# Kernel tuning notes

Measured on AMD Instinct MI355X. Metric: run time of the kernel, lower is better.

## Reference

```python
import jax, jax.numpy as jnp
import numpy as np

DEPTH, BREADTH, N_HEADS = 6, 1024, 16
D_HEAD = BREADTH // N_HEADS
EPS = 1e-5


def layer_norm(x, g, b):
    m = jnp.mean(x, axis=-1, keepdims=True)
    v = jnp.mean(jnp.square(x - m), axis=-1, keepdims=True)
    return (x - m) * jax.lax.rsqrt(v + EPS) * g + b


def setup_inputs() -> dict:
    key = jax.random.key(0)
    ks = jax.random.split(key, 16)
    B, S, Dm, Dff = 4, 1024, BREADTH, 4 * BREADTH
    s = 0.02
    return {
        "x": jax.random.normal(ks[0], (B, S, Dm), dtype=jnp.float32),
        "mask": jnp.ones((B, S, S), dtype=jnp.int32),
        "wq": s * jax.random.normal(ks[1], (DEPTH, Dm, Dm), dtype=jnp.float32),
        "bq": jnp.zeros((DEPTH, Dm), dtype=jnp.float32),
        "wk": s * jax.random.normal(ks[2], (DEPTH, Dm, Dm), dtype=jnp.float32),
        "bk": jnp.zeros((DEPTH, Dm), dtype=jnp.float32),
        "wv": s * jax.random.normal(ks[3], (DEPTH, Dm, Dm), dtype=jnp.float32),
        "bv": jnp.zeros((DEPTH, Dm), dtype=jnp.float32),
        "wo": s * jax.random.normal(ks[4], (DEPTH, Dm, Dm), dtype=jnp.float32),
        "bo": jnp.zeros((DEPTH, Dm), dtype=jnp.float32),
        "w1": s * jax.random.normal(ks[5], (DEPTH, Dm, Dff), dtype=jnp.float32),
        "b1": jnp.zeros((DEPTH, Dff), dtype=jnp.float32),
        "w2": s * jax.random.normal(ks[6], (DEPTH, Dff, Dm), dtype=jnp.float32),
        "b2": jnp.zeros((DEPTH, Dm), dtype=jnp.float32),
        "ln1g": jnp.ones((DEPTH, Dm), dtype=jnp.float32),
        "ln1b": jnp.zeros((DEPTH, Dm), dtype=jnp.float32),
        "ln2g": jnp.ones((DEPTH, Dm), dtype=jnp.float32),
        "ln2b": jnp.zeros((DEPTH, Dm), dtype=jnp.float32),
        "lnfg": jnp.ones((Dm,), dtype=jnp.float32),
        "lnfb": jnp.zeros((Dm,), dtype=jnp.float32),
    }


def reference(x, mask, wq, bq, wk, bk, wv, bv, wo, bo, w1, b1, w2, b2,
              ln1g, ln1b, ln2g, ln2b, lnfg, lnfb):
    B, S, Dm = x.shape
    scale = 1.0 / jnp.sqrt(jnp.float32(D_HEAD))
    neg = jnp.float32(-1e9)
    mask_b = (mask == 0)[:, None]  # [B,1,S,S]

    def split_heads(t):  # [B,S,Dm] -> [B,H,S,d]
        return t.reshape(B, S, N_HEADS, D_HEAD).transpose(0, 2, 1, 3)

    for i in range(DEPTH):
        xn1 = layer_norm(x, ln1g[i], ln1b[i])  # attention branch input
        xn2 = layer_norm(x, ln2g[i], ln2b[i])  # FFN branch input (pre-attention, per original)

        q = split_heads(xn1 @ wq[i] + bq[i])
        k = split_heads(xn1 @ wk[i] + bk[i])
        v = split_heads(xn1 @ wv[i] + bv[i])
        scores = jnp.einsum("bhqd,bhkd->bhqk", q, k) * scale
        scores = jnp.where(mask_b, neg, scores)
        attn = jax.nn.softmax(scores, axis=-1)
        ctx = jnp.einsum("bhqk,bhkd->bhqd", attn, v)
        ctx = ctx.transpose(0, 2, 1, 3).reshape(B, S, Dm)
        x = x + (ctx @ wo[i] + bo[i])

        h = jax.nn.relu(xn2 @ w1[i] + b1[i])
        x = x + (h @ w2[i] + b2[i])

    return layer_norm(x, lnfg, lnfb)
```

## Files before the change

kernel.cpp:

```cpp
#include <hip/hip_runtime.h>
#include <hip/hip_bf16.h>
#include <stdint.h>

#define DEPTH 6
#define DM 1024
#define DFF 4096
#define NH 16
#define DH 64
#define BATCH 4
#define SEQ 1024
#define NTOK (BATCH*SEQ)
#define QKVLD 3072

using bf16x8 = __attribute__((ext_vector_type(8))) short;
using f32x4  = __attribute__((ext_vector_type(4))) float;
typedef unsigned short u16;

__device__ __forceinline__ u16 f2bf(float f) {
  union { float f; uint32_t u; } v; v.f = f;
  return (u16)((v.u + 0x7FFFu + ((v.u >> 16) & 1u)) >> 16);
}

__device__ __forceinline__ void async16(void* lds, const void* g) {
  __builtin_amdgcn_global_load_lds(
      (__attribute__((address_space(1))) void*)(unsigned long long)g,
      (__attribute__((address_space(3))) void*)(unsigned int)(unsigned long long)lds,
      16, 0, 0);
}

#define BARRIER() do { __builtin_amdgcn_s_barrier(); asm volatile("" ::: "memory"); } while (0)

__global__ __launch_bounds__(256)
void prep(const float* __restrict__ wq, const float* __restrict__ wk,
          const float* __restrict__ wv, const float* __restrict__ wo,
          const float* __restrict__ w1, const float* __restrict__ w2,
          const float* __restrict__ bq, const float* __restrict__ bk,
          const float* __restrict__ bv,
          u16* __restrict__ wqkvT, u16* __restrict__ woT,
          u16* __restrict__ w1T, u16* __restrict__ w2T,
          float* __restrict__ bqkv) {
  const int bid = blockIdx.x;
  if (bid >= 12288) {
    const int t = (bid - 12288) * 256 + threadIdx.x;
    bqkv[t] = t < 1024 ? bq[t] : (t < 2048 ? bk[t - 1024] : bv[t - 2048]);
    return;
  }
  const float* w; u16* wt; int K, N, tile;
  if (bid < 3072)      { const int r = bid >> 10;
                         w = r == 0 ? wq : (r == 1 ? wk : wv);
                         wt = wqkvT + (size_t)r * 1024 * 1024; K = 1024; N = 1024; tile = bid & 1023; }
  else if (bid < 4096) { w = wo; wt = woT; K = 1024; N = 1024; tile = bid - 3072; }
  else if (bid < 8192) { w = w1; wt = w1T; K = 1024; N = 4096; tile = bid - 4096; }
  else                 { w = w2; wt = w2T; K = 4096; N = 1024; tile = bid - 8192; }
  const int ntn = N >> 5;
  const int k0 = (tile / ntn) << 5, n0 = (tile % ntn) << 5;

  __shared__ u16 t[32][33];
  const int tx = threadIdx.x & 31, ty = threadIdx.x >> 5;
  #pragma unroll
  for (int r = ty; r < 32; r += 8)
    t[r][tx] = f2bf(w[(size_t)(k0 + r) * N + n0 + tx]);
  __syncthreads();
  #pragma unroll
  for (int r = ty; r < 32; r += 8)
    wt[(size_t)(n0 + r) * K + k0 + tx] = t[tx][r];
}

__global__ __launch_bounds__(256)
void vtrans(const u16* __restrict__ qkv, u16* __restrict__ vt) {
  __shared__ u16 t[64][72];
  const int s0 = blockIdx.x * 64, c0 = blockIdx.y * 64, b = blockIdx.z;
  const int r = threadIdx.x >> 2, cq = threadIdx.x & 3;
  const u16* src = qkv + ((size_t)(b * SEQ + s0 + r)) * QKVLD + 2048 + c0 + cq * 16;
  *(bf16x8*)&t[r][cq * 16]     = *(const bf16x8*)(src);
  *(bf16x8*)&t[r][cq * 16 + 8] = *(const bf16x8*)(src + 8);
  __syncthreads();
  bf16x8 a, bvec;
  #pragma unroll
  for (int i = 0; i < 8; i++) a[i] = (short)t[cq * 16 + i][r];
  #pragma unroll
  for (int i = 0; i < 8; i++) bvec[i] = (short)t[cq * 16 + 8 + i][r];
  u16* dst = vt + ((size_t)(b * 1024 + c0 + r)) * SEQ + s0 + cq * 16;
  *(bf16x8*)dst = a;
  *(bf16x8*)(dst + 8) = bvec;
}

__global__ void flags_init(int* flags) {
  if (threadIdx.x < BATCH) flags[threadIdx.x] = 1;
}
__global__ void mask_flags(const int* __restrict__ mask, int* __restrict__ flags) {
  const size_t n = (size_t)BATCH * SEQ * SEQ;
  for (size_t i = (size_t)blockIdx.x * 256 + threadIdx.x; i < n; i += (size_t)gridDim.x * 256)
    if (mask[i] == 0) flags[i / ((size_t)SEQ * SEQ)] = 0;
}

__global__ __launch_bounds__(256)
void ln_dual(const float* __restrict__ x,
             const float* __restrict__ g1, const float* __restrict__ b1v,
             const float* __restrict__ g2, const float* __restrict__ b2v,
             u16* __restrict__ o1, u16* __restrict__ o2) {
  const int row = blockIdx.x, tid = threadIdx.x;
  const float4 v = ((const float4*)(x + (size_t)row * DM))[tid];
  float s = v.x + v.y + v.z + v.w;
  float sq = v.x*v.x + v.y*v.y + v.z*v.z + v.w*v.w;
  #pragma unroll
  for (int o = 32; o; o >>= 1) { s += __shfl_xor(s, o); sq += __shfl_xor(sq, o); }
  __shared__ float red[8];
  const int lane = tid & 63, w = tid >> 6;
  if (lane == 0) { red[w] = s; red[4 + w] = sq; }
  __syncthreads();
  s = red[0] + red[1] + red[2] + red[3];
  sq = red[4] + red[5] + red[6] + red[7];
  const float mean = s * (1.0f / DM);
  const float rinv = rsqrtf(sq * (1.0f / DM) - mean * mean + 1e-5f);
  const float4 G1 = ((const float4*)g1)[tid], B1 = ((const float4*)b1v)[tid];
  const float4 G2 = ((const float4*)g2)[tid], B2 = ((const float4*)b2v)[tid];
  const float n0 = (v.x - mean) * rinv, n1 = (v.y - mean) * rinv;
  const float n2 = (v.z - mean) * rinv, n3 = (v.w - mean) * rinv;
  ushort4 a, bb;
  a.x = f2bf(n0*G1.x + B1.x); a.y = f2bf(n1*G1.y + B1.y);
  a.z = f2bf(n2*G1.z + B1.z); a.w = f2bf(n3*G1.w + B1.w);
  bb.x = f2bf(n0*G2.x + B2.x); bb.y = f2bf(n1*G2.y + B2.y);
  bb.z = f2bf(n2*G2.z + B2.z); bb.w = f2bf(n3*G2.w + B2.w);
  ((ushort4*)(o1 + (size_t)row * DM))[tid] = a;
  ((ushort4*)(o2 + (size_t)row * DM))[tid] = bb;
}

__global__ __launch_bounds__(256)
void ln_final(const float* __restrict__ x, const float* __restrict__ g,
              const float* __restrict__ b, float* __restrict__ out) {
  const int row = blockIdx.x, tid = threadIdx.x;
  const float4 v = ((const float4*)(x + (size_t)row * DM))[tid];
  float s = v.x + v.y + v.z + v.w;
  float sq = v.x*v.x + v.y*v.y + v.z*v.z + v.w*v.w;
  #pragma unroll
  for (int o = 32; o; o >>= 1) { s += __shfl_xor(s, o); sq += __shfl_xor(sq, o); }
  __shared__ float red[8];
  const int lane = tid & 63, w = tid >> 6;
  if (lane == 0) { red[w] = s; red[4 + w] = sq; }
  __syncthreads();
  s = red[0] + red[1] + red[2] + red[3];
  sq = red[4] + red[5] + red[6] + red[7];
  const float mean = s * (1.0f / DM);
  const float rinv = rsqrtf(sq * (1.0f / DM) - mean * mean + 1e-5f);
  const float4 G = ((const float4*)g)[tid], B = ((const float4*)b)[tid];
  float4 o;
  o.x = (v.x - mean) * rinv * G.x + B.x;
  o.y = (v.y - mean) * rinv * G.y + B.y;
  o.z = (v.z - mean) * rinv * G.z + B.z;
  o.w = (v.w - mean) * rinv * G.w + B.w;
  ((float4*)(out + (size_t)row * DM))[tid] = o;
}

template<int EPI, int SPLITK>
__global__ __launch_bounds__(512, 2)
void gemm256(const u16* __restrict__ A, const u16* __restrict__ BT,
             const float* __restrict__ bias,
             u16* __restrict__ Cb, float* __restrict__ Cf,
             int M, int N, int K) {
  __shared__ u16 lds[65536];
  char* ldsb = (char*)lds;
  const int tid = threadIdx.x;
  const int lane = tid & 63;
  const int wid = tid >> 6;
  const int wm = wid >> 2, wn = wid & 3;
  const int l16 = lane & 15, lhi = lane >> 4;
  const int xr = (l16 & 7) << 4;

  const int ntn = N >> 8;
  const int ntiles = (M >> 8) * ntn;
  const int nwg = ntiles * SPLITK;
  int wg = (int)blockIdx.x;
  if ((nwg & 7) == 0) { const int q = nwg >> 3; wg = (wg & 7) * q + (wg >> 3); }
  const int ks = wg / ntiles;
  const int tile = wg % ntiles;
  const int tm = tile / ntn, tn = tile % ntn;
  const int KS = K / SPLITK;
  const int k0 = ks * KS;
  const int NT = KS >> 6;

  const u16 *aS[4], *bS[4];
  #pragma unroll
  for (int g = 0; g < 4; g++) {
    const int D  = tid * 16 + g * 8192;
    const int Dh = D & 16383, half = D >> 14;
    const int Ds = Dh ^ (((Dh >> 7) & 7) << 4);
    const int grow = half * 128 + (Ds >> 7);
    const int gcol = (Ds & 127) >> 1;
    aS[g] = A  + (size_t)(tm * 256 + grow) * K + k0 + gcol;
    bS[g] = BT + (size_t)(tn * 256 + grow) * K + k0 + gcol;
  }
  auto stageA = [&](int buf, int t) {
    #pragma unroll
    for (int g = 0; g < 4; g++)
      async16(ldsb + buf * 32768 + g * 8192 + tid * 16, aS[g] + t * 64);
  };
  auto stageB = [&](int buf, int t) {
    #pragma unroll
    for (int g = 0; g < 4; g++)
      async16(ldsb + 65536 + buf * 32768 + g * 8192 + tid * 16, bS[g] + t * 64);
  };
  auto ldA = [&](int buf, int mq, int m, int kk) -> bf16x8 {
    const int L = (mq * 64 + m * 16 + l16) * 128 + kk * 64 + lhi * 16;
    return *(const bf16x8*)(ldsb + buf * 32768 + wm * 16384 + (L ^ xr));
  };
  auto ldB = [&](int buf, int nq, int n, int kk) -> bf16x8 {
    const int L = ((wn & 1) * 64 + nq * 32 + n * 16 + l16) * 128 + kk * 64 + lhi * 16;
    return *(const bf16x8*)(ldsb + 65536 + buf * 32768 + (wn >> 1) * 16384 + (L ^ xr));
  };

  f32x4 acc[8][4];
  #pragma unroll
  for (int m = 0; m < 8; m++)
    #pragma unroll
    for (int n = 0; n < 4; n++)
      #pragma unroll
      for (int j = 0; j < 4; j++) acc[m][n][j] = 0.0f;

  stageA(0, 0); stageB(0, 0);
  stageA(1, 1); stageB(1, 1);
  asm volatile("s_waitcnt vmcnt(8)" ::: "memory");
  BARRIER();

  bf16x8 a[4][2], b0[2][2], b1[2][2];
  for (int t = 0; t < NT; ++t) {
    const int buf = t & 1;
    #pragma unroll
    for (int m = 0; m < 4; m++)
      #pragma unroll
      for (int kk = 0; kk < 2; kk++) a[m][kk] = ldA(buf, 0, m, kk);
    #pragma unroll
    for (int n = 0; n < 2; n++)
      #pragma unroll
      for (int kk = 0; kk < 2; kk++) b0[n][kk] = ldB(buf, 0, n, kk);
    BARRIER();
    asm volatile("s_waitcnt lgkmcnt(0)" ::: "memory");
    __builtin_amdgcn_s_setprio(1);
    #pragma unroll
    for (int m = 0; m < 4; m++)
      #pragma unroll
      for (int n = 0; n < 2; n++)
        #pragma unroll
        for (int kk = 0; kk < 2; kk++)
          acc[m][n] = __builtin_amdgcn_mfma_f32_16x16x32_bf16(a[m][kk], b0[n][kk], acc[m][n], 0, 0, 0);
    __builtin_amdgcn_s_setprio(0);
    BARRIER();
    #pragma unroll
    for (int n = 0; n < 2; n++)
      #pragma unroll
      for (int kk = 0; kk < 2; kk++) b1[n][kk] = ldB(buf, 1, n, kk);
    BARRIER();
    asm volatile("s_waitcnt lgkmcnt(0)" ::: "memory");
    __builtin_amdgcn_s_setprio(1);
    #pragma unroll
    for (int m = 0; m < 4; m++)
      #pragma unroll
      for (int n = 0; n < 2; n++)
        #pragma unroll
        for (int kk = 0; kk < 2; kk++)
          acc[m][2 + n] = __builtin_amdgcn_mfma_f32_16x16x32_bf16(a[m][kk], b1[n][kk], acc[m][2 + n], 0, 0, 0);
    __builtin_amdgcn_s_setprio(0);
    BARRIER();
    #pragma unroll
    for (int m = 0; m < 4; m++)
      #pragma unroll
      for (int kk = 0; kk < 2; kk++) a[m][kk] = ldA(buf, 1, m, kk);
    if (t + 2 < NT) stageB(buf, t + 2);
    BARRIER();
    asm volatile("s_waitcnt lgkmcnt(0)" ::: "memory");
    __builtin_amdgcn_s_setprio(1);
    #pragma unroll
    for (int m = 0; m < 4; m++)
      #pragma unroll
      for (int n = 0; n < 2; n++)
        #pragma unroll
        for (int kk = 0; kk < 2; kk++)
          acc[4 + m][2 + n] = __builtin_amdgcn_mfma_f32_16x16x32_bf16(a[m][kk], b1[n][kk], acc[4 + m][2 + n], 0, 0, 0);
    __builtin_amdgcn_s_setprio(0);
    BARRIER();
    if (t + 2 < NT) stageA(buf, t + 2);
    BARRIER();
    __builtin_amdgcn_s_setprio(1);
    #pragma unroll
    for (int m = 0; m < 4; m++)
      #pragma unroll
      for (int n = 0; n < 2; n++)
        #pragma unroll
        for (int kk = 0; kk < 2; kk++)
          acc[4 + m][n] = __builtin_amdgcn_mfma_f32_16x16x32_bf16(a[m][kk], b0[n][kk], acc[4 + m][n], 0, 0, 0);
    __builtin_amdgcn_s_setprio(0);
    if (t + 1 < NT) {
      if (t + 2 < NT) asm volatile("s_waitcnt vmcnt(8)" ::: "memory");
      else            asm volatile("s_waitcnt vmcnt(0)" ::: "memory");
      BARRIER();
    }
  }

  const int row0 = tm * 256 + wm * 128 + lhi * 4;
  const int col0 = tn * 256 + wn * 64 + l16;
  #pragma unroll
  for (int ng = 0; ng < 4; ng++) {
    const int col = col0 + ng * 16;
    const float bv = bias[col];
    #pragma unroll
    for (int mg = 0; mg < 8; mg++) {
      #pragma unroll
      for (int j = 0; j < 4; j++) {
        const int row = row0 + mg * 16 + j;
        float v = acc[mg][ng][j];
        if constexpr (EPI == 2 && SPLITK > 1) {
          if (ks == 0) v += bv;
          unsafeAtomicAdd(&Cf[(size_t)row * N + col], v);
        } else {
          v += bv;
          if constexpr (EPI == 1) v = fmaxf(v, 0.0f);
          if constexpr (EPI <= 1) Cb[(size_t)row * N + col] = f2bf(v);
          else                    Cf[(size_t)row * N + col] += v;
        }
      }
    }
  }
}

template<int EPI, int BN>
__global__ __launch_bounds__(256)
void gemm_bt(const u16* __restrict__ A, const u16* __restrict__ BT,
             const float* __restrict__ bias,
             u16* __restrict__ Cb, float* __restrict__ Cf,
             int M, int N, int K) {
  constexpr int WCn = BN / 64;
  constexpr int WR  = 4 / WCn;
  constexpr int MF  = 8 / WR;
  constexpr int WRS = 128 / WR;
  constexpr int ASZ = 128 * 32;
  constexpr int BSZ = BN * 32;
  __shared__ u16 As[2 * ASZ];
  __shared__ u16 Bs[2 * BSZ];
  const int tid = threadIdx.x;
  const int lane = tid & 63, wave = tid >> 6;
  const int wr = wave / WCn, wc = wave % WCn;
  const int l16 = lane & 15, lhi = lane >> 4;

  const int ntn = N / BN;
  const int nwg = (M >> 7) * ntn;
  int wg = (int)blockIdx.x;
  if ((nwg & 7) == 0) { const int q = nwg >> 3; wg = (wg & 7) * q + (wg >> 3); }
  const int tm = wg / ntn, tn = wg % ntn;

  const int srow = tid >> 2, sc = (tid & 3) * 8;
  const u16* Ag0 = A  + (size_t)(tm * 128 + srow) * K + sc;
  const u16* Bg0 = BT + (size_t)(tn * BN + srow) * K + sc;
  const size_t rstep = (size_t)64 * K;

  auto stage = [&](int buf, int k0) {
    async16(As + buf * ASZ + tid * 8, Ag0 + k0);
    async16(As + buf * ASZ + 2048 + tid * 8, Ag0 + rstep + k0);
    async16(Bs + buf * BSZ + tid * 8, Bg0 + k0);
    if constexpr (BN == 128) async16(Bs + buf * BSZ + 2048 + tid * 8, Bg0 + rstep + k0);
  };

  f32x4 acc[MF][4];
  #pragma unroll
  for (int m = 0; m < MF; m++)
    #pragma unroll
    for (int n = 0; n < 4; n++)
      #pragma unroll
      for (int j = 0; j < 4; j++) acc[m][n][j] = 0.0f;

  stage(0, 0);
  __syncthreads();
  int cur = 0;
  for (int k0 = 0; k0 < K; k0 += 32) {
    if (k0 + 32 < K) stage(cur ^ 1, k0 + 32);
    const u16* Ab = As + cur * ASZ;
    const u16* Bb = Bs + cur * BSZ;
    bf16x8 af[MF], bfv[4];
    #pragma unroll
    for (int m = 0; m < MF; m++)
      af[m] = *(const bf16x8*)&Ab[(wr * WRS + m * 16 + l16) * 32 + lhi * 8];
    #pragma unroll
    for (int n = 0; n < 4; n++)
      bfv[n] = *(const bf16x8*)&Bb[(wc * 64 + n * 16 + l16) * 32 + lhi * 8];
    #pragma unroll
    for (int m = 0; m < MF; m++)
      #pragma unroll
      for (int n = 0; n < 4; n++)
        acc[m][n] = __builtin_amdgcn_mfma_f32_16x16x32_bf16(af[m], bfv[n], acc[m][n], 0, 0, 0);
    __syncthreads();
    cur ^= 1;
  }

  const int row0 = tm * 128 + wr * WRS + lhi * 4;
  const int col0 = tn * BN + wc * 64 + l16;
  #pragma unroll
  for (int n = 0; n < 4; n++) {
    const int col = col0 + n * 16;
    const float bv = bias[col];
    #pragma unroll
    for (int m = 0; m < MF; m++) {
      #pragma unroll
      for (int j = 0; j < 4; j++) {
        const int row = row0 + m * 16 + j;
        float v = acc[m][n][j] + bv;
        if constexpr (EPI == 1) v = fmaxf(v, 0.0f);
        if constexpr (EPI <= 1) Cb[(size_t)row * N + col] = f2bf(v);
        else                    Cf[(size_t)row * N + col] += v;
      }
    }
  }
}

__global__ __launch_bounds__(256, 4)
void attn(const u16* __restrict__ QKV, const u16* __restrict__ VTg,
          u16* __restrict__ Octx,
          const int* __restrict__ mask, const int* __restrict__ flags) {
  __shared__ u16 Ks[2 * 64 * 64];
  __shared__ u16 VTs[2 * 64 * 64];
  __shared__ u16 Ps[4 * 16 * 64];
  const int tid = threadIdx.x, lane = tid & 63, wv = tid >> 6;
  const int l16 = lane & 15, lhi = lane >> 4;
  const int bid = blockIdx.x;
  const int pair = bid >> 4, qblk = bid & 15;
  const int b = pair >> 4, h = pair & 15;
  const int hoff = h * DH;
  const int q0 = qblk * 64 + wv * 16;
  const size_t tokbase = (size_t)b * SEQ;
  const size_t vbase = ((size_t)b * 1024 + hoff) * SEQ;

  bf16x8 qf[2];
  #pragma unroll
  for (int ds = 0; ds < 2; ds++)
    qf[ds] = *(const bf16x8*)&QKV[(tokbase + q0 + l16) * QKVLD + hoff + ds * 32 + lhi * 8];

  f32x4 oacc[4];
  #pragma unroll
  for (int nt = 0; nt < 4; nt++)
    #pragma unroll
    for (int j = 0; j < 4; j++) oacc[nt][j] = 0.0f;
  float mrun = -1e30f, lrun = 0.0f;

  const int allone = flags[b];
  char* PwB = (char*)(Ps + wv * (16 * 64));
  const int xw = (l16 & 7) << 4;

  const int srow0 = tid >> 3, scb0 = (tid & 7) ^ (srow0 & 7);
  const int srow1 = (tid + 256) >> 3, scb1 = (tid & 7) ^ (srow1 & 7);
  const int shfl_src = (lane & 48) + ((lane >> 4) << 2);

  auto stage = [&](int buf, int kt) {
    async16((char*)Ks + buf * 8192 + tid * 16,
            &QKV[(tokbase + kt + srow0) * QKVLD + 1024 + hoff + scb0 * 8]);
    async16((char*)Ks + buf * 8192 + 4096 + tid * 16,
            &QKV[(tokbase + kt + srow1) * QKVLD + 1024 + hoff + scb1 * 8]);
    async16((char*)VTs + buf * 8192 + tid * 16,
            &VTg[vbase + (size_t)srow0 * SEQ + kt + scb0 * 8]);
    async16((char*)VTs + buf * 8192 + 4096 + tid * 16,
            &VTg[vbase + (size_t)srow1 * SEQ + kt + scb1 * 8]);
  };

  stage(0, 0);
  __syncthreads();
  int cur = 0;
  for (int kt = 0; kt < SEQ; kt += 64) {
    if (kt + 64 < SEQ) stage(cur ^ 1, kt + 64);
    char* KsB = (char*)Ks + cur * 8192;
    char* VTB = (char*)VTs + cur * 8192;

    f32x4 sacc[4];
    #pragma unroll
    for (int nt = 0; nt < 4; nt++)
      #pragma unroll
      for (int j = 0; j < 4; j++) sacc[nt][j] = 0.0f;
    #pragma unroll
    for (int ds = 0; ds < 2; ds++) {
      bf16x8 kf[4];
      #pragma unroll
      for (int nt = 0; nt < 4; nt++) {
        const int rk = nt * 16 + l16;
        kf[nt] = *(const bf16x8*)(KsB + ((rk * 128 + ds * 64 + lhi * 16) ^ ((rk & 7) << 4)));
      }
      #pragma unroll
      for (int nt = 0; nt < 4; nt++)
        sacc[nt] = __builtin_amdgcn_mfma_f32_16x16x32_bf16(kf[nt], qf[ds], sacc[nt], 0, 0, 0);
    }
    #pragma unroll
    for (int nt = 0; nt < 4; nt++)
      #pragma unroll
      for (int j = 0; j < 4; j++) sacc[nt][j] *= 0.125f;

    if (!allone) {
      const int qg = q0 + l16;
      #pragma unroll
      for (int nt = 0; nt < 4; nt++)
        #pragma unroll
        for (int j = 0; j < 4; j++) {
          const int kc = kt + nt * 16 + lhi * 4 + j;
          if (mask[(tokbase + qg) * SEQ + kc] == 0) sacc[nt][j] = -1e9f;
        }
    }

    float tmax = -1e30f;
    #pragma unroll
    for (int nt = 0; nt < 4; nt++)
      #pragma unroll
      for (int j = 0; j < 4; j++) tmax = fmaxf(tmax, sacc[nt][j]);
    tmax = fmaxf(tmax, __shfl_xor(tmax, 16));
    tmax = fmaxf(tmax, __shfl_xor(tmax, 32));
    const float mnew = fmaxf(mrun, tmax);
    const float corr = __expf(mrun - mnew);
    float p[4][4];
    float tsum = 0.0f;
    #pragma unroll
    for (int nt = 0; nt < 4; nt++)
      #pragma unroll
      for (int j = 0; j < 4; j++) { p[nt][j] = __expf(sacc[nt][j] - mnew); tsum += p[nt][j]; }
    tsum += __shfl_xor(tsum, 16);
    tsum += __shfl_xor(tsum, 32);
    lrun = lrun * corr + tsum;
    mrun = mnew;

    #pragma unroll
    for (int nt = 0; nt < 4; nt++) {
      const uint32_t lo = (uint32_t)f2bf(p[nt][0]) | ((uint32_t)f2bf(p[nt][1]) << 16);
      const uint32_t hi = (uint32_t)f2bf(p[nt][2]) | ((uint32_t)f2bf(p[nt][3]) << 16);
      *(uint64_t*)(PwB + ((l16 * 128 + nt * 32 + lhi * 8) ^ xw)) =
          (uint64_t)lo | ((uint64_t)hi << 32);
    }

    float cj[4];
    #pragma unroll
    for (int j = 0; j < 4; j++) cj[j] = __shfl(corr, shfl_src + j);
    #pragma unroll
    for (int nt = 0; nt < 4; nt++)
      #pragma unroll
      for (int j = 0; j < 4; j++) oacc[nt][j] *= cj[j];

    #pragma unroll
    for (int ksl = 0; ksl < 2; ksl++) {
      const bf16x8 pf = *(const bf16x8*)(PwB + ((l16 * 128 + ksl * 64 + lhi * 16) ^ xw));
      #pragma unroll
      for (int nt = 0; nt < 4; nt++) {
        const int dr = nt * 16 + l16;
        const bf16x8 vf = *(const bf16x8*)(VTB + ((dr * 128 + ksl * 64 + lhi * 16) ^ ((dr & 7) << 4)));
        oacc[nt] = __builtin_amdgcn_mfma_f32_16x16x32_bf16(pf, vf, oacc[nt], 0, 0, 0);
      }
    }
    __syncthreads();
    cur ^= 1;
  }

  const float linv = 1.0f / lrun;
  float lj[4];
  #pragma unroll
  for (int j = 0; j < 4; j++) lj[j] = __shfl(linv, shfl_src + j);
  #pragma unroll
  for (int j = 0; j < 4; j++) {
    const size_t rowg = (tokbase + q0 + lhi * 4 + j) * DM + hoff;
    #pragma unroll
    for (int nt = 0; nt < 4; nt++)
      Octx[rowg + nt * 16 + l16] = f2bf(oacc[nt][j] * lj[j]);
  }
}

extern "C" void kernel_launch(void* const* d_in, const int* in_sizes, int n_in,
                              void* d_out, int out_size, void* d_ws, size_t ws_size,
                              hipStream_t stream) {
  const float* x    = (const float*)d_in[0];
  const int*   mask = (const int*)d_in[1];
  const float* wq = (const float*)d_in[2];
  const float* bq = (const float*)d_in[3];
  const float* wk = (const float*)d_in[4];
  const float* bk = (const float*)d_in[5];
  const float* wvp = (const float*)d_in[6];
  const float* bv = (const float*)d_in[7];
  const float* wo = (const float*)d_in[8];
  const float* bo = (const float*)d_in[9];
  const float* w1 = (const float*)d_in[10];
  const float* b1 = (const float*)d_in[11];
  const float* w2 = (const float*)d_in[12];
  const float* b2 = (const float*)d_in[13];
  const float* ln1g = (const float*)d_in[14];
  const float* ln1b = (const float*)d_in[15];
  const float* ln2g = (const float*)d_in[16];
  const float* ln2b = (const float*)d_in[17];
  const float* lnfg = (const float*)d_in[18];
  const float* lnfb = (const float*)d_in[19];

  char* ws = (char*)d_ws;
  float* xbuf = (float*)(ws);
  u16* xn1  = (u16*)(ws + ((size_t)16 << 20));
  u16* xn2  = (u16*)(ws + ((size_t)24 << 20));
  u16* qkv  = (u16*)(ws + ((size_t)32 << 20));
  u16* ctx  = (u16*)(ws + ((size_t)56 << 20));
  u16* hb   = (u16*)(ws + ((size_t)32 << 20));
  u16* wqkvT= (u16*)(ws + ((size_t)64 << 20));
  u16* woT  = (u16*)(ws + ((size_t)70 << 20));
  u16* w1T  = (u16*)(ws + ((size_t)72 << 20));
  u16* w2T  = (u16*)(ws + ((size_t)80 << 20));
  u16* vT   = (u16*)(ws + ((size_t)88 << 20));
  float* bqkv = (float*)(ws + ((size_t)96 << 20));
  int* flags  = (int*)(ws + ((size_t)96 << 20) + 65536);

  hipMemcpyAsync(xbuf, x, (size_t)NTOK * DM * sizeof(float),
                 hipMemcpyDeviceToDevice, stream);
  flags_init<<<1, 64, 0, stream>>>(flags);
  mask_flags<<<1024, 256, 0, stream>>>(mask, flags);

  auto wgs64 = [](int M, int N) { return dim3((unsigned)((M >> 7) * (N >> 6))); };

  for (int i = 0; i < DEPTH; i++) {
    prep<<<12300, 256, 0, stream>>>(
        wq  + (size_t)i * DM * DM,  wk + (size_t)i * DM * DM,
        wvp + (size_t)i * DM * DM,  wo + (size_t)i * DM * DM,
        w1  + (size_t)i * DM * DFF, w2 + (size_t)i * DFF * DM,
        bq + i * DM, bk + i * DM, bv + i * DM,
        wqkvT, woT, w1T, w2T, bqkv);

    ln_dual<<<NTOK, 256, 0, stream>>>(xbuf, ln1g + i * DM, ln1b + i * DM,
                                      ln2g + i * DM, ln2b + i * DM, xn1, xn2);

    gemm256<0, 1><<<dim3(192), 512, 0, stream>>>(xn1, wqkvT, bqkv, qkv, nullptr,
                                                 NTOK, QKVLD, DM);
    vtrans<<<dim3(16, 16, 4), 256, 0, stream>>>(qkv, vT);

    attn<<<1024, 256, 0, stream>>>(qkv, vT, ctx, mask, flags);

    gemm_bt<2, 64><<<wgs64(NTOK, DM), 256, 0, stream>>>(ctx, woT, bo + i * DM, nullptr, xbuf,
                                                        NTOK, DM, DM);
    gemm256<1, 1><<<dim3(256), 512, 0, stream>>>(xn2, w1T, b1 + i * DFF, hb, nullptr,
                                                 NTOK, DFF, DM);
    gemm256<2, 4><<<dim3(256), 512, 0, stream>>>(hb, w2T, b2 + i * DM, nullptr, xbuf,
                                                 NTOK, DM, DFF);
  }

  ln_final<<<NTOK, 256, 0, stream>>>(xbuf, lnfg, lnfb, (float*)d_out);
}
```

Baseline: 1.591 ms.

## Restage gemm256 loads in finer half-tile chunks interleaved with MFMA phases

Rewrites the gemm256 main loop to stage A and B tiles in half-tile pieces, each issued right after the LDS region it replaces has been consumed, and unrolls the K loop by two so each buffer has fixed offsets. The goal is to start global-to-LDS prefetch earlier and overlap it more evenly with the four MFMA phases, with a matching vmcnt(6) wait. The LDS layout changes so A and B sub-blocks are contiguous per quarter, and the occupancy hint of 2 blocks per CU is dropped from launch bounds. The loop assumes an even tile count, and the epilogue's non-split-K path now always writes bf16, which removes the Cf accumulation branch.

```diff
diff --git a/kernel.cpp b/kernel.cpp
--- a/kernel.cpp
+++ b/kernel.cpp
@@ -29,6 +29,9 @@
 }
 
 #define BARRIER() do { __builtin_amdgcn_s_barrier(); asm volatile("" ::: "memory"); } while (0)
+#define LGKM0()   asm volatile("s_waitcnt lgkmcnt(0)" ::: "memory")
+#define VMCNT6()  asm volatile("s_waitcnt vmcnt(6)" ::: "memory")
+#define VMCNT0()  asm volatile("s_waitcnt vmcnt(0)" ::: "memory")
 
 __global__ __launch_bounds__(256)
 void prep(const float* __restrict__ wq, const float* __restrict__ wk,
@@ -153,16 +156,14 @@
 }
 
 template<int EPI, int SPLITK>
-__global__ __launch_bounds__(512, 2)
+__global__ __launch_bounds__(512)
 void gemm256(const u16* __restrict__ A, const u16* __restrict__ BT,
              const float* __restrict__ bias,
              u16* __restrict__ Cb, float* __restrict__ Cf,
              int M, int N, int K) {
   __shared__ u16 lds[65536];
-  char* ldsb = (char*)lds;
-  const int tid = threadIdx.x;
-  const int lane = tid & 63;
-  const int wid = tid >> 6;
+  char* AB = (char*)lds;
+  const int tid = threadIdx.x, lane = tid & 63, wid = tid >> 6;
   const int wm = wid >> 2, wn = wid & 3;
   const int l16 = lane & 15, lhi = lane >> 4;
   const int xr = (l16 & 7) << 4;
@@ -172,41 +173,39 @@
   const int nwg = ntiles * SPLITK;
   int wg = (int)blockIdx.x;
   if ((nwg & 7) == 0) { const int q = nwg >> 3; wg = (wg & 7) * q + (wg >> 3); }
-  const int ks = wg / ntiles;
-  const int tile = wg % ntiles;
+  const int ks = wg / ntiles, tile = wg % ntiles;
   const int tm = tile / ntn, tn = tile % ntn;
-  const int KS = K / SPLITK;
-  const int k0 = ks * KS;
-  const int NT = KS >> 6;
-
-  const u16 *aS[4], *bS[4];
-  #pragma unroll
-  for (int g = 0; g < 4; g++) {
-    const int D  = tid * 16 + g * 8192;
-    const int Dh = D & 16383, half = D >> 14;
-    const int Ds = Dh ^ (((Dh >> 7) & 7) << 4);
-    const int grow = half * 128 + (Ds >> 7);
-    const int gcol = (Ds & 127) >> 1;
-    aS[g] = A  + (size_t)(tm * 256 + grow) * K + k0 + gcol;
-    bS[g] = BT + (size_t)(tn * 256 + grow) * K + k0 + gcol;
-  }
-  auto stageA = [&](int buf, int t) {
-    #pragma unroll
-    for (int g = 0; g < 4; g++)
-      async16(ldsb + buf * 32768 + g * 8192 + tid * 16, aS[g] + t * 64);
+  const int KS = K / SPLITK, kbase = ks * KS, NT = KS >> 6;
+
+  const int sr = tid >> 3;
+  const int scb = ((tid & 7) * 16) ^ ((sr & 7) << 4);
+  const u16 *aS[2], *bS[2];
+  #pragma unroll
+  for (int i = 0; i < 2; i++) {
+    aS[i] = A  + (size_t)(tm * 256 + i * 128 + sr) * K + kbase + (scb >> 1);
+    bS[i] = BT + (size_t)(tn * 256 + (i * 2 + (tid >> 8)) * 64 + (sr & 31)) * K + kbase + (scb >> 1);
+  }
+  auto stageA = [&](int buf, int h, int t) {
+    #pragma unroll
+    for (int i = 0; i < 2; i++)
+      async16(AB + buf * 32768 + h * 16384 + i * 8192 + tid * 16,
+              aS[i] + (size_t)h * 64 * K + t * 64);
   };
-  auto stageB = [&](int buf, int t) {
-    #pragma unroll
-    for (int g = 0; g < 4; g++)
-      async16(ldsb + 65536 + buf * 32768 + g * 8192 + tid * 16, bS[g] + t * 64);
+  auto stageB = [&](int buf, int g, int t) {
+    #pragma unroll
+    for (int i = 0; i < 2; i++)
+      async16(AB + 65536 + buf * 32768 + g * 16384 + i * 8192 + tid * 16,
+              bS[i] + (size_t)g * 32 * K + t * 64);
   };
-  auto ldA = [&](int buf, int mq, int m, int kk) -> bf16x8 {
-    const int L = (mq * 64 + m * 16 + l16) * 128 + kk * 64 + lhi * 16;
-    return *(const bf16x8*)(ldsb + buf * 32768 + wm * 16384 + (L ^ xr));
+  auto ldA = [&](int buf, int m, int kk) -> bf16x8 {
+    const int r = (m & 3) * 16 + l16;
+    return *(const bf16x8*)(AB + buf * 32768 + (m >> 2) * 16384 + wm * 8192 +
+                            r * 128 + ((kk * 64 + lhi * 16) ^ xr));
   };
-  auto ldB = [&](int buf, int nq, int n, int kk) -> bf16x8 {
-    const int L = ((wn & 1) * 64 + nq * 32 + n * 16 + l16) * 128 + kk * 64 + lhi * 16;
-    return *(const bf16x8*)(ldsb + 65536 + buf * 32768 + (wn >> 1) * 16384 + (L ^ xr));
+  auto ldB = [&](int buf, int n, int kk) -> bf16x8 {
+    const int r = (n & 1) * 16 + l16;
+    return *(const bf16x8*)(AB + 65536 + buf * 32768 + (n >> 1) * 16384 + wn * 4096 +
+                            r * 128 + ((kk * 64 + lhi * 16) ^ xr));
   };
 
   f32x4 acc[8][4];
@@ -217,84 +216,93 @@
       #pragma unroll
       for (int j = 0; j < 4; j++) acc[m][n][j] = 0.0f;
 
-  stageA(0, 0); stageB(0, 0);
-  stageA(1, 1); stageB(1, 1);
-  asm volatile("s_waitcnt vmcnt(8)" ::: "memory");
+  stageA(0, 0, 0); stageB(0, 0, 0); stageB(0, 1, 0); stageA(0, 1, 0);
+  stageA(1, 0, 1); stageB(1, 0, 1); stageB(1, 1, 1);
+  VMCNT6();
   BARRIER();
 
   bf16x8 a[4][2], b0[2][2], b1[2][2];
-  for (int t = 0; t < NT; ++t) {
-    const int buf = t & 1;
-    #pragma unroll
-    for (int m = 0; m < 4; m++)
-      #pragma unroll
-      for (int kk = 0; kk < 2; kk++) a[m][kk] = ldA(buf, 0, m, kk);
-    #pragma unroll
-    for (int n = 0; n < 2; n++)
-      #pragma unroll
-      for (int kk = 0; kk < 2; kk++) b0[n][kk] = ldB(buf, 0, n, kk);
-    BARRIER();
-    asm volatile("s_waitcnt lgkmcnt(0)" ::: "memory");
-    __builtin_amdgcn_s_setprio(1);
-    #pragma unroll
-    for (int m = 0; m < 4; m++)
-      #pragma unroll
-      for (int n = 0; n < 2; n++)
-        #pragma unroll
-        for (int kk = 0; kk < 2; kk++)
-          acc[m][n] = __builtin_amdgcn_mfma_f32_16x16x32_bf16(a[m][kk], b0[n][kk], acc[m][n], 0, 0, 0);
-    __builtin_amdgcn_s_setprio(0);
-    BARRIER();
-    #pragma unroll
-    for (int n = 0; n < 2; n++)
-      #pragma unroll
-      for (int kk = 0; kk < 2; kk++) b1[n][kk] = ldB(buf, 1, n, kk);
-    BARRIER();
-    asm volatile("s_waitcnt lgkmcnt(0)" ::: "memory");
-    __builtin_amdgcn_s_setprio(1);
-    #pragma unroll
-    for (int m = 0; m < 4; m++)
-      #pragma unroll
-      for (int n = 0; n < 2; n++)
-        #pragma unroll
-        for (int kk = 0; kk < 2; kk++)
-          acc[m][2 + n] = __builtin_amdgcn_mfma_f32_16x16x32_bf16(a[m][kk], b1[n][kk], acc[m][2 + n], 0, 0, 0);
-    __builtin_amdgcn_s_setprio(0);
-    BARRIER();
-    #pragma unroll
-    for (int m = 0; m < 4; m++)
-      #pragma unroll
-      for (int kk = 0; kk < 2; kk++) a[m][kk] = ldA(buf, 1, m, kk);
-    if (t + 2 < NT) stageB(buf, t + 2);
-    BARRIER();
-    asm volatile("s_waitcnt lgkmcnt(0)" ::: "memory");
-    __builtin_amdgcn_s_setprio(1);
-    #pragma unroll
-    for (int m = 0; m < 4; m++)
-      #pragma unroll
-      for (int n = 0; n < 2; n++)
-        #pragma unroll
-        for (int kk = 0; kk < 2; kk++)
-          acc[4 + m][2 + n] = __builtin_amdgcn_mfma_f32_16x16x32_bf16(a[m][kk], b1[n][kk], acc[4 + m][2 + n], 0, 0, 0);
-    __builtin_amdgcn_s_setprio(0);
-    BARRIER();
-    if (t + 2 < NT) stageA(buf, t + 2);
-    BARRIER();
-    __builtin_amdgcn_s_setprio(1);
-    #pragma unroll
-    for (int m = 0; m < 4; m++)
-      #pragma unroll
-      for (int n = 0; n < 2; n++)
-        #pragma unroll
-        for (int kk = 0; kk < 2; kk++)
-          acc[4 + m][n] = __builtin_amdgcn_mfma_f32_16x16x32_bf16(a[m][kk], b0[n][kk], acc[4 + m][n], 0, 0, 0);
-    __builtin_amdgcn_s_setprio(0);
-    if (t + 1 < NT) {
-      if (t + 2 < NT) asm volatile("s_waitcnt vmcnt(8)" ::: "memory");
-      else            asm volatile("s_waitcnt vmcnt(0)" ::: "memory");
-      BARRIER();
-    }
-  }
+
+#define MFMA16(MO, NO, AR, BR)                                                   \
+  __builtin_amdgcn_s_setprio(1);                                                \
+  _Pragma("unroll")                                                             \
+  for (int mm = 0; mm < 4; mm++)                                                \
+    _Pragma("unroll")                                                           \
+    for (int nn = 0; nn < 2; nn++)                                              \
+      _Pragma("unroll")                                                         \
+      for (int kk = 0; kk < 2; kk++)                                            \
+        acc[MO + mm][NO + nn] = __builtin_amdgcn_mfma_f32_16x16x32_bf16(        \
+            AR[mm][kk], BR[nn][kk], acc[MO + mm][NO + nn], 0, 0, 0);            \
+  __builtin_amdgcn_s_setprio(0);
+
+  for (int T = 0; T < NT; T += 2) {
+    #pragma unroll
+    for (int mm = 0; mm < 4; mm++)
+      #pragma unroll
+      for (int kk = 0; kk < 2; kk++) a[mm][kk] = ldA(0, mm, kk);
+    #pragma unroll
+    for (int nn = 0; nn < 2; nn++)
+      #pragma unroll
+      for (int kk = 0; kk < 2; kk++) b0[nn][kk] = ldB(0, nn, kk);
+    stageA(1, 1, T + 1);
+    BARRIER(); LGKM0();
+    MFMA16(0, 0, a, b0)
+    BARRIER();
+    #pragma unroll
+    for (int nn = 0; nn < 2; nn++)
+      #pragma unroll
+      for (int kk = 0; kk < 2; kk++) b1[nn][kk] = ldB(0, 2 + nn, kk);
+    if (T + 2 < NT) stageA(0, 0, T + 2);
+    BARRIER(); LGKM0();
+    MFMA16(0, 2, a, b1)
+    BARRIER();
+    #pragma unroll
+    for (int mm = 0; mm < 4; mm++)
+      #pragma unroll
+      for (int kk = 0; kk < 2; kk++) a[mm][kk] = ldA(0, 4 + mm, kk);
+    if (T + 2 < NT) stageB(0, 0, T + 2);
+    BARRIER(); LGKM0();
+    MFMA16(4, 2, a, b1)
+    BARRIER();
+    if (T + 2 < NT) stageB(0, 1, T + 2);
+    BARRIER();
+    MFMA16(4, 0, a, b0)
+    if (T + 2 < NT) { VMCNT6(); } else { VMCNT0(); }
+    BARRIER();
+    #pragma unroll
+    for (int mm = 0; mm < 4; mm++)
+      #pragma unroll
+      for (int kk = 0; kk < 2; kk++) a[mm][kk] = ldA(1, mm, kk);
+    #pragma unroll
+    for (int nn = 0; nn < 2; nn++)
+      #pragma unroll
+      for (int kk = 0; kk < 2; kk++) b0[nn][kk] = ldB(1, nn, kk);
+    if (T + 2 < NT) stageA(0, 1, T + 2);
+    BARRIER(); LGKM0();
+    MFMA16(0, 0, a, b0)
+    BARRIER();
+    #pragma unroll
+    for (int nn = 0; nn < 2; nn++)
+      #pragma unroll
+      for (int kk = 0; kk < 2; kk++) b1[nn][kk] = ldB(1, 2 + nn, kk);
+    if (T + 3 < NT) stageA(1, 0, T + 3);
+    BARRIER(); LGKM0();
+    MFMA16(0, 2, a, b1)
+    BARRIER();
+    #pragma unroll
+    for (int mm = 0; mm < 4; mm++)
+      #pragma unroll
+      for (int kk = 0; kk < 2; kk++) a[mm][kk] = ldA(1, 4 + mm, kk);
+    if (T + 3 < NT) stageB(1, 0, T + 3);
+    BARRIER(); LGKM0();
+    MFMA16(4, 2, a, b1)
+    BARRIER();
+    if (T + 3 < NT) stageB(1, 1, T + 3);
+    BARRIER();
+    MFMA16(4, 0, a, b0)
+    if (T + 2 < NT) { VMCNT6(); BARRIER(); }
+  }
+#undef MFMA16
 
   const int row0 = tm * 256 + wm * 128 + lhi * 4;
   const int col0 = tn * 256 + wn * 64 + l16;
@@ -314,8 +322,7 @@
         } else {
           v += bv;
           if constexpr (EPI == 1) v = fmaxf(v, 0.0f);
-          if constexpr (EPI <= 1) Cb[(size_t)row * N + col] = f2bf(v);
-          else                    Cf[(size_t)row * N + col] += v;
+          Cb[(size_t)row * N + col] = f2bf(v);
         }
       }
     }
@@ -625,8 +632,9 @@
 
     attn<<<1024, 256, 0, stream>>>(qkv, vT, ctx, mask, flags);
 
-    gemm_bt<2, 64><<<wgs64(NTOK, DM), 256, 0, stream>>>(ctx, woT, bo + i * DM, nullptr, xbuf,
-                                                        NTOK, DM, DM);
+    gemm_bt<2, 64><<<wgs64(NTOK, DM), 256, 0, stream>>>(
+        ctx, woT, bo + i * DM, nullptr, xbuf, NTOK, DM, DM);
+
     gemm256<1, 1><<<dim3(256), 512, 0, stream>>>(xn2, w1T, b1 + i * DFF, hb, nullptr,
                                                  NTOK, DFF, DM);
     gemm256<2, 4><<<dim3(256), 512, 0, stream>>>(hb, w2T, b2 + i * DM, nullptr, xbuf,
```

Measured after the change: 1.543 ms. 3.0% less time.
